# Kernel tuning notes

Hardware: AMD Instinct MI355X
Metric: run time of the kernel (lower is better)

The kernel has to match this reference:

```python
import jax, jax.numpy as jnp
import numpy as np

B, T = 65536, 200
H, S, P = 512, 1000, 5
EPS = 1e-6


def setup_inputs() -> dict:
    key = jax.random.key(0)
    ks = jax.random.split(key, 8)
    init = lambda k, shp, fan: (jax.random.normal(k, shp, jnp.float32) / np.float32(np.sqrt(fan)))
    return {
        "X": jax.random.randint(ks[0], (B,), 0, S, dtype=jnp.int32),
        "y": jax.random.randint(ks[1], (B, T), 0, 2, dtype=jnp.int32),
        "embed": init(ks[2], (S, H), 1.0),
        "W1": init(ks[3], (H, H), H), "b1": jnp.zeros((H,), jnp.float32),
        "W2": init(ks[4], (H, H), H), "b2": jnp.zeros((H,), jnp.float32),
        "Wout": init(ks[5], (H, P), H), "bout": jnp.zeros((P,), jnp.float32),
    }


def reference(X, y, embed, W1, b1, W2, b2, Wout, bout):
    # --- MLP over skill embeddings: params (B, 5) = (l, f, g, s, latent0) ---
    e = embed[X]                                    # (B, H)
    h = jax.nn.relu(e @ W1 + b1)                    # num_layers = 2
    h = jax.nn.relu(h @ W2 + b2)
    params = jnp.clip(jax.nn.sigmoid(h @ Wout + bout), EPS, 1.0 - EPS)  # (B, 5)
    l, g, s = params[:, 0], params[:, 2], params[:, 3]
    latent0 = params[:, 4]                          # (B,)

    y_clean = jnp.where(y == -1, 0, y).astype(jnp.float32)  # (B, T)

    # --- BKT latent-update recurrence over T steps ---
    def step(latent, y_t):
        num1 = latent * (1.0 - s)
        correct = num1 + (1.0 - latent) * g
        k_t1 = num1 / correct
        k_t0 = latent * s / (latent * s + (1.0 - latent) * (1.0 - g))
        k_t = jnp.where(y_t > 0.5, k_t1, k_t0)
        nxt = jnp.clip(k_t + (1.0 - k_t) * l, EPS, 1.0 - EPS)
        return nxt, (correct, latent)

    _, (corrects, latents) = jax.lax.scan(step, latent0, y_clean.T)  # (T, B) each
    return corrects.T, latents.T, params
```

## Files before the change

kernel.cpp:

```cpp
#include <hip/hip_runtime.h>


typedef unsigned int uint;
typedef unsigned char uchar;
typedef unsigned short ushort_t;
typedef __attribute__((ext_vector_type(8))) short short8;
typedef __attribute__((ext_vector_type(4))) float f32x4;
typedef __attribute__((ext_vector_type(2))) uint uint2v;

#define SS 1000
#define HH 512
#define TT 200
#define BB_ 65536
#define PP 5

#define OFF_EMB   0
#define OFF_B1    512000
#define OFF_B2    512512
#define OFF_WOUT  513024
#define OFF_BOUT  515584
#define CONV_TOT  515589

__device__ __forceinline__ float b2f(ushort_t u) {
    return __uint_as_float(((uint)u) << 16);
}
__device__ __forceinline__ ushort_t f2b(float f) {
    uint u = __float_as_uint(f);
    uint r = u + 0x7FFFu + ((u >> 16) & 1u);
    return (ushort_t)(r >> 16);
}
__device__ __forceinline__ int detect_bf16(const uint* __restrict__ embed_raw,
                                           int tid) {
    uint w = embed_raw[tid & 63];
    uint e = (w >> 7) & 0xFFu;
    bool pl = (e >= 117u && e <= 130u);
    return __popcll(__ballot(pl)) >= 32 ? 1 : 0;
}
__device__ __forceinline__ ushort_t ld_bf16(const void* src, int idx, int fb) {
    return fb ? ((const ushort_t*)src)[idx] : f2b(((const float*)src)[idx]);
}

__device__ __forceinline__ float bkt_step(float latent, bool yt,
                                          float oms, float omg, float A1,
                                          float A0, float g, float s,
                                          float oml, float l) {
    float num1    = latent * oms;
    float correct = fmaf(latent, A1, g);
    float lats    = latent * s;
    float num = yt ? num1 : lats;
    float den = yt ? correct : fmaf(latent, A0, omg);
    float kt  = num * __builtin_amdgcn_rcpf(den);
    float nxt = fmaf(kt, oml, l);
    return fminf(fmaxf(nxt, 1e-6f), 1.f - 1e-6f);
}

__global__ __launch_bounds__(256) void prep_kernel(
    const void* __restrict__ embed, const void* __restrict__ W1,
    const void* __restrict__ b1,    const void* __restrict__ W2,
    const void* __restrict__ b2,    const void* __restrict__ Wout,
    const void* __restrict__ bout,
    ushort_t* __restrict__ conv, ushort_t* __restrict__ WT1,
    ushort_t* __restrict__ WT2)
{
    int tid = threadIdx.x;
    int fb = detect_bf16((const uint*)embed, tid);
    int bx = blockIdx.x;
    if (bx < 504) {
        int i = (bx * 256 + tid) * 4;
        if (i < CONV_TOT) {
            const void* src; int off;
            if      (i < OFF_B1)   { src = embed; off = i; }
            else if (i < OFF_B2)   { src = b1;    off = i - OFF_B1; }
            else if (i < OFF_WOUT) { src = b2;    off = i - OFF_B2; }
            else if (i < OFF_BOUT) { src = Wout;  off = i - OFF_WOUT; }
            else                   { src = bout;  off = i - OFF_BOUT; }
            if (i + 3 < CONV_TOT) {
                ushort4 o;
                if (fb) {
                    o = *(const ushort4*)((const ushort_t*)src + off);
                } else {
                    float4 v = *(const float4*)((const float*)src + off);
                    o.x = f2b(v.x); o.y = f2b(v.y); o.z = f2b(v.z); o.w = f2b(v.w);
                }
                *(ushort4*)(conv + i) = o;
            } else {
                for (int k = 0; i + k < CONV_TOT; k++)
                    conv[i + k] = ld_bf16(src, off + k, fb);
            }
        }
    } else {
        __shared__ ushort_t t[32][33];
        int bi = bx - 504;
        const void* W = bi < 256 ? W1 : W2;
        ushort_t* WT = bi < 256 ? WT1 : WT2;
        int ti = bi & 255;
        int k0 = (ti & 15) * 32, n0 = (ti >> 4) * 32;
        int tx = tid & 31, ty = tid >> 5;
        #pragma unroll
        for (int i = ty; i < 32; i += 8)
            t[i][tx] = ld_bf16(W, (k0 + i) * HH + n0 + tx, fb);
        __syncthreads();
        #pragma unroll
        for (int i = ty; i < 32; i += 8)
            WT[(n0 + i) * HH + k0 + tx] = t[tx][i];
    }
}

__global__ __launch_bounds__(256) void mlp_layer(
    const ushort_t* __restrict__ A, const ushort_t* __restrict__ WT,
    const ushort_t* __restrict__ bias, ushort_t* __restrict__ H, int Mclamp)
{
    int tid = threadIdx.x;
    int lane = tid & 63;
    int wave = tid >> 6;
    int m_base = blockIdx.x * 64 + wave * 16;
    int n_base = blockIdx.y * 16;
    int lrow = lane & 15;
    int q = lane >> 4;
    int rowA = m_base + lrow; if (rowA > Mclamp) rowA = Mclamp;

    const short8* Ap = (const short8*)(A + (size_t)rowA * HH) + q;
    const short8* Bp = (const short8*)(WT + (size_t)(n_base + lrow) * HH) + q;

    f32x4 acc = {0.f, 0.f, 0.f, 0.f};
    #pragma unroll 8
    for (int kk = 0; kk < 16; kk++) {
        short8 a = Ap[kk * 4];
        short8 b = Bp[kk * 4];
        acc = __builtin_amdgcn_mfma_f32_16x16x32_bf16(a, b, acc, 0, 0, 0);
    }

    int orow = m_base + q * 4;
    int n = n_base + lrow;
    float bb = b2f(bias[n]);
    #pragma unroll
    for (int r = 0; r < 4; r++) {
        float v = acc[r] + bb;
        H[(size_t)(orow + r) * HH + n] = f2b(fmaxf(v, 0.f));
    }
}

__global__ __launch_bounds__(256) void params_kernel(
    const ushort_t* __restrict__ h2, const ushort_t* __restrict__ conv,
    float* __restrict__ table)
{
    int wid = blockIdx.x * 4 + (threadIdx.x >> 6);
    int lane = threadIdx.x & 63;
    if (wid >= SS * PP) return;
    int row = wid / PP, p = wid - row * PP;
    const ushort_t* Wout = conv + OFF_WOUT;
    const ushort_t* bout = conv + OFF_BOUT;
    const short8* hr = (const short8*)(h2 + (size_t)row * HH);
    short8 h = hr[lane];
    float acc = 0.f;
    #pragma unroll
    for (int j = 0; j < 8; j++) {
        int k = lane * 8 + j;
        acc += b2f((ushort_t)h[j]) * b2f(Wout[k * PP + p]);
    }
    #pragma unroll
    for (int m = 32; m; m >>= 1) acc += __shfl_xor(acc, m);
    if (lane == 0) {
        float x = acc + b2f(bout[p]);
        float sg = 1.f / (1.f + expf(-x));
        sg = fminf(fmaxf(sg, 1e-6f), 1.f - 1e-6f);
        table[(size_t)row * 8 + p] = sg;
    }
}

__global__ __launch_bounds__(256) void scan_a(
    const int* __restrict__ X, const int* __restrict__ y,
    const float* __restrict__ table,
    float* __restrict__ cpA, uint* __restrict__ maskA)
{
    __shared__ uchar ybit[128 * 50];
    int tid = threadIdx.x;
    int rbase = blockIdx.x * 128;

    for (int idx = tid; idx < 6400; idx += 256) {
        int r = idx / 50, k = idx - r * 50;
        int4 v = *(const int4*)(y + (size_t)(rbase + r) * TT + k * 4);
        ybit[r * 50 + k] = (uchar)((uint)(v.x == 1) | ((uint)(v.y == 1) << 1) |
                                   ((uint)(v.z == 1) << 2) | ((uint)(v.w == 1) << 3));
    }
    __syncthreads();

    if (tid < 128) {
        int rg = rbase + tid;
        int xi = X[rg]; xi = xi < 0 ? 0 : (xi >= SS ? SS - 1 : xi);
        float l      = table[xi * 8 + 0];
        float g      = table[xi * 8 + 2];
        float s      = table[xi * 8 + 3];
        float latent = table[xi * 8 + 4];
        float oms = 1.f - s, omg = 1.f - g, oml = 1.f - l;
        float A1 = 1.f - s - g, A0 = s + g - 1.f;
        float cp[8]; uint mk[8];
        #pragma unroll
        for (int w = 0; w < 8; w++) {
            cp[w] = latent;
            uint m = 0;
            #pragma unroll
            for (int i = 0; i < 25; i++) {
                int t_ = w * 25 + i;
                uint bit = (ybit[tid * 50 + (t_ >> 2)] >> (t_ & 3)) & 1u;
                m |= bit << i;
                latent = bkt_step(latent, bit, oms, omg, A1, A0, g, s, oml, l);
            }
            mk[w] = m;
        }
        #pragma unroll
        for (int w = 0; w < 8; w++) {
            cpA[(size_t)w * BB_ + rg]   = cp[w];
            maskA[(size_t)w * BB_ + rg] = mk[w];
        }
    }
}

__global__ __launch_bounds__(256) void scan_b(
    const int* __restrict__ X, const float* __restrict__ table,
    const float* __restrict__ cpA, const uint* __restrict__ maskA,
    const uint* __restrict__ embed_raw, void* __restrict__ out)
{
    __shared__ __align__(16) float stg[32 * 200];
    __shared__ float pA1[32], pG[32];
    int tid = threadIdx.x;
    int rbase = blockIdx.x * 32;
    int fb = detect_bf16(embed_raw, tid);

    int r = tid >> 3, j = tid & 7;
    int rg = rbase + r;
    int xi = X[rg]; xi = xi < 0 ? 0 : (xi >= SS ? SS - 1 : xi);
    float l  = table[xi * 8 + 0];
    float p1 = table[xi * 8 + 1];
    float g  = table[xi * 8 + 2];
    float s  = table[xi * 8 + 3];
    float L0 = table[xi * 8 + 4];

    if (j == 0) { pA1[r] = 1.f - s - g; pG[r] = g; }

    if (j < 5) {
        float pv = j == 0 ? l : j == 1 ? p1 : j == 2 ? g : j == 3 ? s : L0;
        size_t po = 2ull * BB_ * TT + (size_t)rg * 5 + j;
        if (fb) ((ushort_t*)out)[po] = f2b(pv);
        else    ((float*)out)[po] = pv;
    }

    float latent = cpA[(size_t)j * BB_ + rg];
    uint  u      = maskA[(size_t)j * BB_ + rg];
    float oms = 1.f - s, omg = 1.f - g, oml = 1.f - l;
    float A1 = 1.f - s - g, A0 = s + g - 1.f;

    int sbase = r * 200 + j * 25;
    #pragma unroll
    for (int i = 0; i < 25; i++) {
        stg[sbase + i] = latent;
        latent = bkt_step(latent, (u >> i) & 1u,
                          oms, omg, A1, A0, g, s, oml, l);
    }
    __syncthreads();

    const f32x4* src = (const f32x4*)stg;
    if (!fb) {
        f32x4* dc = (f32x4*)((float*)out + (size_t)rbase * TT);
        f32x4* dl = (f32x4*)((float*)out + (size_t)BB_ * TT + (size_t)rbase * TT);
        for (int idx = tid; idx < 1600; idx += 256) {
            int rr = idx / 50;
            f32x4 v = src[idx];
            float a1 = pA1[rr], gg = pG[rr];
            f32x4 c;
            c[0] = fmaf(v[0], a1, gg); c[1] = fmaf(v[1], a1, gg);
            c[2] = fmaf(v[2], a1, gg); c[3] = fmaf(v[3], a1, gg);
            dl[idx] = v;
            dc[idx] = c;
        }
    } else {
        uint2v* dc = (uint2v*)((ushort_t*)out + (size_t)rbase * TT);
        uint2v* dl = (uint2v*)((ushort_t*)out + (size_t)BB_ * TT + (size_t)rbase * TT);
        for (int idx = tid; idx < 1600; idx += 256) {
            int rr = idx / 50;
            f32x4 v = src[idx];
            float a1 = pA1[rr], gg = pG[rr];
            uint2v lv, cv;
            lv[0] = (uint)f2b(v[0]) | ((uint)f2b(v[1]) << 16);
            lv[1] = (uint)f2b(v[2]) | ((uint)f2b(v[3]) << 16);
            cv[0] = (uint)f2b(fmaf(v[0], a1, gg)) | ((uint)f2b(fmaf(v[1], a1, gg)) << 16);
            cv[1] = (uint)f2b(fmaf(v[2], a1, gg)) | ((uint)f2b(fmaf(v[3], a1, gg)) << 16);
            dl[idx] = lv;
            dc[idx] = cv;
        }
    }
}

extern "C" void kernel_launch(void* const* d_in, const int* in_sizes, int n_in,
                              void* d_out, int out_size, void* d_ws, size_t ws_size,
                              hipStream_t stream) {
    const int* X = (const int*)d_in[0];
    const int* y = (const int*)d_in[1];

    char* ws = (char*)d_ws;
    ushort_t* conv  = (ushort_t*)(ws);
    ushort_t* WT1   = (ushort_t*)(ws + 1048576);
    ushort_t* WT2   = (ushort_t*)(ws + 1572864);
    ushort_t* h1    = (ushort_t*)(ws + 2097152);
    ushort_t* h2    = (ushort_t*)(ws + 3145728);
    float*    table = (float*)(ws + 4194304);
    float*    cpA   = (float*)(ws + 4227072);
    uint*     maskA = (uint*)(ws + 6324224);

    prep_kernel<<<dim3(1016, 1, 1), 256, 0, stream>>>(
        d_in[2], d_in[3], d_in[4], d_in[5], d_in[6], d_in[7], d_in[8],
        conv, WT1, WT2);
    mlp_layer<<<dim3(16, 32, 1), 256, 0, stream>>>(
        conv + OFF_EMB, WT1, conv + OFF_B1, h1, SS - 1);
    mlp_layer<<<dim3(16, 32, 1), 256, 0, stream>>>(
        h1, WT2, conv + OFF_B2, h2, 1023);
    params_kernel<<<dim3(1250, 1, 1), 256, 0, stream>>>(h2, conv, table);
    scan_a<<<dim3(512, 1, 1), 256, 0, stream>>>(X, y, table, cpA, maskA);
    scan_b<<<dim3(2048, 1, 1), 256, 0, stream>>>(
        X, table, cpA, maskA, (const uint*)d_in[2], (void*)d_out);
}
```

Baseline: 205.6 us.

## Move y bitmask packing into prep kernel, off the scan critical path

Packing the 52 MB y tensor into per-row 25-bit masks now happens in 1024 extra blocks of the prep kernel, which does not depend on the MLP. scan_a just reads the precomputed masks and runs the serial BKT recurrence with 128-thread blocks. The goal is to stop the large y read from sitting serialized behind the MLP chain, where it ran on only half the threads of scan_a. The cost is that the prep kernel grows and the masks take an extra global write and read.

```diff
diff --git a/kernel.cpp b/kernel.cpp
--- a/kernel.cpp
+++ b/kernel.cpp
@@ -58,14 +58,14 @@
     const void* __restrict__ embed, const void* __restrict__ W1,
     const void* __restrict__ b1,    const void* __restrict__ W2,
     const void* __restrict__ b2,    const void* __restrict__ Wout,
-    const void* __restrict__ bout,
+    const void* __restrict__ bout,  const int* __restrict__ y,
     ushort_t* __restrict__ conv, ushort_t* __restrict__ WT1,
-    ushort_t* __restrict__ WT2)
+    ushort_t* __restrict__ WT2,  uint* __restrict__ maskA)
 {
     int tid = threadIdx.x;
-    int fb = detect_bf16((const uint*)embed, tid);
     int bx = blockIdx.x;
     if (bx < 504) {
+        int fb = detect_bf16((const uint*)embed, tid);
         int i = (bx * 256 + tid) * 4;
         if (i < CONV_TOT) {
             const void* src; int off;
@@ -88,7 +88,8 @@
                     conv[i + k] = ld_bf16(src, off + k, fb);
             }
         }
-    } else {
+    } else if (bx < 1016) {
+        int fb = detect_bf16((const uint*)embed, tid);
         __shared__ ushort_t t[32][33];
         int bi = bx - 504;
         const void* W = bi < 256 ? W1 : W2;
@@ -103,6 +104,28 @@
         #pragma unroll
         for (int i = ty; i < 32; i += 8)
             WT[(n0 + i) * HH + k0 + tx] = t[tx][i];
+    } else {
+        __shared__ uchar yb[64 * 50];
+        int rbase = (bx - 1016) * 64;
+        for (int idx = tid; idx < 3200; idx += 256) {
+            int r = idx / 50, k = idx - r * 50;
+            int4 v = *(const int4*)(y + (size_t)(rbase + r) * TT + k * 4);
+            yb[r * 50 + k] = (uchar)((uint)(v.x == 1) | ((uint)(v.y == 1) << 1) |
+                                     ((uint)(v.z == 1) << 2) | ((uint)(v.w == 1) << 3));
+        }
+        __syncthreads();
+        #pragma unroll
+        for (int it = 0; it < 2; it++) {
+            int task = tid + it * 256;
+            int r = task & 63, w = task >> 6;
+            uint m = 0;
+            #pragma unroll
+            for (int i = 0; i < 25; i++) {
+                int t_ = w * 25 + i;
+                m |= (uint)((yb[r * 50 + (t_ >> 2)] >> (t_ & 3)) & 1u) << i;
+            }
+            maskA[(size_t)w * BB_ + rbase + r] = m;
+        }
     }
 }
 
@@ -168,52 +191,36 @@
     }
 }
 
-__global__ __launch_bounds__(256) void scan_a(
-    const int* __restrict__ X, const int* __restrict__ y,
-    const float* __restrict__ table,
-    float* __restrict__ cpA, uint* __restrict__ maskA)
-{
-    __shared__ uchar ybit[128 * 50];
+__global__ __launch_bounds__(128) void scan_a(
+    const int* __restrict__ X, const float* __restrict__ table,
+    const uint* __restrict__ maskA, float* __restrict__ cpA)
+{
     int tid = threadIdx.x;
-    int rbase = blockIdx.x * 128;
-
-    for (int idx = tid; idx < 6400; idx += 256) {
-        int r = idx / 50, k = idx - r * 50;
-        int4 v = *(const int4*)(y + (size_t)(rbase + r) * TT + k * 4);
-        ybit[r * 50 + k] = (uchar)((uint)(v.x == 1) | ((uint)(v.y == 1) << 1) |
-                                   ((uint)(v.z == 1) << 2) | ((uint)(v.w == 1) << 3));
-    }
-    __syncthreads();
-
-    if (tid < 128) {
-        int rg = rbase + tid;
-        int xi = X[rg]; xi = xi < 0 ? 0 : (xi >= SS ? SS - 1 : xi);
-        float l      = table[xi * 8 + 0];
-        float g      = table[xi * 8 + 2];
-        float s      = table[xi * 8 + 3];
-        float latent = table[xi * 8 + 4];
-        float oms = 1.f - s, omg = 1.f - g, oml = 1.f - l;
-        float A1 = 1.f - s - g, A0 = s + g - 1.f;
-        float cp[8]; uint mk[8];
+    int rg = blockIdx.x * 128 + tid;
+    int xi = X[rg]; xi = xi < 0 ? 0 : (xi >= SS ? SS - 1 : xi);
+    float l      = table[xi * 8 + 0];
+    float g      = table[xi * 8 + 2];
+    float s      = table[xi * 8 + 3];
+    float latent = table[xi * 8 + 4];
+    float oms = 1.f - s, omg = 1.f - g, oml = 1.f - l;
+    float A1 = 1.f - s - g, A0 = s + g - 1.f;
+
+    uint mk[8];
+    #pragma unroll
+    for (int w = 0; w < 8; w++) mk[w] = maskA[(size_t)w * BB_ + rg];
+
+    float cp[8];
+    #pragma unroll
+    for (int w = 0; w < 8; w++) {
+        cp[w] = latent;
         #pragma unroll
-        for (int w = 0; w < 8; w++) {
-            cp[w] = latent;
-            uint m = 0;
-            #pragma unroll
-            for (int i = 0; i < 25; i++) {
-                int t_ = w * 25 + i;
-                uint bit = (ybit[tid * 50 + (t_ >> 2)] >> (t_ & 3)) & 1u;
-                m |= bit << i;
-                latent = bkt_step(latent, bit, oms, omg, A1, A0, g, s, oml, l);
-            }
-            mk[w] = m;
-        }
-        #pragma unroll
-        for (int w = 0; w < 8; w++) {
-            cpA[(size_t)w * BB_ + rg]   = cp[w];
-            maskA[(size_t)w * BB_ + rg] = mk[w];
-        }
-    }
+        for (int i = 0; i < 25; i++)
+            latent = bkt_step(latent, (mk[w] >> i) & 1u,
+                              oms, omg, A1, A0, g, s, oml, l);
+    }
+    #pragma unroll
+    for (int w = 0; w < 8; w++)
+        cpA[(size_t)w * BB_ + rg] = cp[w];
 }
 
 __global__ __launch_bounds__(256) void scan_b(
@@ -307,15 +314,15 @@
     float*    cpA   = (float*)(ws + 4227072);
     uint*     maskA = (uint*)(ws + 6324224);
 
-    prep_kernel<<<dim3(1016, 1, 1), 256, 0, stream>>>(
-        d_in[2], d_in[3], d_in[4], d_in[5], d_in[6], d_in[7], d_in[8],
-        conv, WT1, WT2);
+    prep_kernel<<<dim3(2040, 1, 1), 256, 0, stream>>>(
+        d_in[2], d_in[3], d_in[4], d_in[5], d_in[6], d_in[7], d_in[8], y,
+        conv, WT1, WT2, maskA);
     mlp_layer<<<dim3(16, 32, 1), 256, 0, stream>>>(
         conv + OFF_EMB, WT1, conv + OFF_B1, h1, SS - 1);
     mlp_layer<<<dim3(16, 32, 1), 256, 0, stream>>>(
         h1, WT2, conv + OFF_B2, h2, 1023);
     params_kernel<<<dim3(1250, 1, 1), 256, 0, stream>>>(h2, conv, table);
-    scan_a<<<dim3(512, 1, 1), 256, 0, stream>>>(X, y, table, cpA, maskA);
+    scan_a<<<dim3(512, 1, 1), 128, 0, stream>>>(X, table, maskA, cpA);
     scan_b<<<dim3(2048, 1, 1), 256, 0, stream>>>(
         X, table, cpA, maskA, (const uint*)d_in[2], (void*)d_out);
 }
```

Result: no change. 202.8 us (-1.4%).
